# Optimization experiments

Measured on AMD Instinct MI355X. Metric: run time of the kernel, lower is better.

The kernel has to match this reference:

```python
import jax, jax.numpy as jnp
import numpy as np


def dht(x):
    # Discrete Hartley transform along last axis: DHT(x) = Re(FFT) - Im(FFT)
    X = jnp.fft.fft(x, axis=-1)
    return (X.real - X.imag).astype(x.dtype)


def idht(x):
    # Inverse DHT = DHT / N
    n = x.shape[-1]
    return dht(x) / n


def setup_inputs() -> dict:
    key = jax.random.key(0)
    k1, k2 = jax.random.split(key)
    B, Cin, Cout, N, M = 16, 64, 64, 16384, 64
    x = jax.random.normal(k1, (B, Cin, N), dtype=jnp.float32)
    scale = 1.0 / (Cin * Cout)
    weights1 = scale * jax.random.uniform(k2, (Cout, Cin, M), dtype=jnp.float32)
    return {"x": x, "weights1": weights1, "modes1": M}


def reference(x, weights1, modes1):
    # x: [B, Cin, N]; weights1: [Cout, Cin, M]
    B, Cin, N = x.shape
    Cout = weights1.shape[0]
    x_ht = dht(x)                                  # [B, Cin, N]
    # Mode-wise channel contraction on the first `modes1` Hartley modes
    low = jnp.einsum('bim,oim->bom', x_ht[:, :, :modes1], weights1)  # [B, Cout, M]
    out_ht = jnp.zeros((B, Cout, N), dtype=x.dtype).at[:, :, :modes1].set(low)
    return idht(out_ht)                            # [B, Cout, N]
```

## Files before the change

### kernel.cpp

```cpp
#include <hip/hip_runtime.h>
#include <math.h>

#define N_FFT 16384
#define HALF 8192
#define ROWS 1024
#define KS_A 64
#define KR_A 128
#define CHUNK 32
#define NMASK 16383


__global__ __launch_bounds__(256) void k_tab(float* __restrict__ castab,
                                             float* __restrict__ costab) {
    int i = blockIdx.x * 256 + threadIdx.x;
    double ang = 6.283185307179586476925287 * (double)i / (double)N_FFT;
    double c = cos(ang), s = sin(ang);
    castab[i] = (float)(c + s);
    costab[i] = (float)(2.0 * c);
}

__global__ __launch_bounds__(512, 4) void kA(const float* __restrict__ x,
                                             const float* __restrict__ castab,
                                             const float* __restrict__ costab,
                                             float* __restrict__ partial) {
    const int rb = blockIdx.x & 7;
    const int ks = blockIdx.x >> 3;
    const int rowbase = rb << 7;
    const int kbase = ks * KR_A;

    __shared__ float xs[CHUNK][2][128];

    const int t   = threadIdx.x;
    const int wq  = __builtin_amdgcn_readfirstlane(t >> 6);
    const int lam = t & 63;
    const int c0  = wq * 8;
    const int p   = wq >> 2;
    const int r2  = lam * 2;
    const int mbase = (wq < 4) ? (wq << 4) : (((wq - 4) << 4) + 1);

    float k2[8], cA[8], cB[8];
#pragma unroll
    for (int j = 0; j < 8; ++j) {
        const int m = mbase + 2 * j;
        k2[j] = costab[m];
        cB[j] = castab[((kbase - 1) * m) & NMASK];
        cA[j] = castab[(kbase * m) & NMASK];
    }

    float acc0[8], acc1[8];
#pragma unroll
    for (int j = 0; j < 8; ++j) { acc0[j] = 0.f; acc1[j] = 0.f; }

    for (int ch = 0; ch < KR_A / CHUNK; ++ch) {
        const int k0 = kbase + ch * CHUNK;
        if (ch) __syncthreads();
#pragma unroll
        for (int it = 0; it < 2; ++it) {
            const int idx = it * 512 + t;
            const int r = idx >> 3, kq = idx & 7;
            const float4 a4 = *reinterpret_cast<const float4*>(
                &x[(size_t)(rowbase + r) * N_FFT + k0 + kq * 4]);
            const float4 b4 = *reinterpret_cast<const float4*>(
                &x[(size_t)(rowbase + r) * N_FFT + k0 + kq * 4 + HALF]);
            const int rsw = r ^ (kq << 1);
#pragma unroll
            for (int u = 0; u < 4; ++u) {
                const float a = reinterpret_cast<const float*>(&a4)[u];
                const float b = reinterpret_cast<const float*>(&b4)[u];
                xs[kq * 4 + u][0][rsw] = a + b;
                xs[kq * 4 + u][1][rsw] = a - b;
            }
        }
        __syncthreads();

        for (int k = 0; k < CHUNK; k += 2) {
            {
                const int rd = r2 ^ ((k >> 2) << 1);
                const float2 s2 = *reinterpret_cast<const float2*>(&xs[k][p][rd]);
#pragma unroll
                for (int j = 0; j < 8; ++j) {
                    acc0[j] = fmaf(s2.x, cA[j], acc0[j]);
                    acc1[j] = fmaf(s2.y, cA[j], acc1[j]);
                    cB[j] = fmaf(k2[j], cA[j], -cB[j]);
                }
            }
            {
                const int rd = r2 ^ (((k + 1) >> 2) << 1);
                const float2 s2 = *reinterpret_cast<const float2*>(&xs[k + 1][p][rd]);
#pragma unroll
                for (int j = 0; j < 8; ++j) {
                    acc0[j] = fmaf(s2.x, cB[j], acc0[j]);
                    acc1[j] = fmaf(s2.y, cB[j], acc1[j]);
                    cA[j] = fmaf(k2[j], cB[j], -cA[j]);
                }
            }
        }
    }

#pragma unroll
    for (int i = 0; i < 2; ++i) {
        float* pp = &partial[((size_t)ks << 16) +
                             (size_t)(rowbase + r2 + i) * 64 + c0];
        const float* a = i ? acc1 : acc0;
        *reinterpret_cast<float4*>(pp) =
            make_float4(a[0], a[1], a[2], a[3]);
        *reinterpret_cast<float4*>(pp + 4) =
            make_float4(a[4], a[5], a[6], a[7]);
    }
}

__global__ __launch_bounds__(256) void kR(const float* __restrict__ partial,
                                          float* __restrict__ xh) {
    const int idx = blockIdx.x * 256 + threadIdx.x;
    const int r = idx >> 6, c = idx & 63;
    const int m = (c < 32) ? (2 * c) : (2 * (c - 32) + 1);
    float a0 = 0.f, a1 = 0.f, a2 = 0.f, a3 = 0.f;
#pragma unroll 4
    for (int sp = 0; sp < KS_A; sp += 4) {
        a0 += partial[((size_t)(sp + 0) << 16) + idx];
        a1 += partial[((size_t)(sp + 1) << 16) + idx];
        a2 += partial[((size_t)(sp + 2) << 16) + idx];
        a3 += partial[((size_t)(sp + 3) << 16) + idx];
    }
    xh[(r << 6) + m] = (a0 + a1) + (a2 + a3);
}

__global__ __launch_bounds__(256) void kB(const float* __restrict__ xh,
                                          const float* __restrict__ w,
                                          float* __restrict__ lowT) {
    const int b  = blockIdx.x >> 4;
    const int og = blockIdx.x & 15;
    const int o  = og * 4 + (threadIdx.x >> 6);
    const int m  = threadIdx.x & 63;
    float a0 = 0.f, a1 = 0.f, a2 = 0.f, a3 = 0.f;
#pragma unroll 4
    for (int i = 0; i < 64; i += 4) {
        a0 = fmaf(xh[(size_t)((b * 64 + i + 0) << 6) + m], w[(size_t)((o * 64 + i + 0) << 6) + m], a0);
        a1 = fmaf(xh[(size_t)((b * 64 + i + 1) << 6) + m], w[(size_t)((o * 64 + i + 1) << 6) + m], a1);
        a2 = fmaf(xh[(size_t)((b * 64 + i + 2) << 6) + m], w[(size_t)((o * 64 + i + 2) << 6) + m], a2);
        a3 = fmaf(xh[(size_t)((b * 64 + i + 3) << 6) + m], w[(size_t)((o * 64 + i + 3) << 6) + m], a3);
    }
    lowT[(size_t)m * ROWS + b * 64 + o] = ((a0 + a1) + (a2 + a3)) * (1.0f / (float)N_FFT);
}

__global__ __launch_bounds__(256, 4) void kC(const float* __restrict__ lowT,
                                             const float* __restrict__ castab,
                                             const float* __restrict__ costab,
                                             float* __restrict__ out) {
    const int rb = blockIdx.x >> 5;
    const int nb = blockIdx.x & 31;
    const int rowbase = rb << 4;
    const int n0 = nb << 8;

    __shared__ float ls[64][16];

    const int t  = threadIdx.x;
    const int rg = __builtin_amdgcn_readfirstlane(t >> 6);
    const int nl = t & 63;
    const int n  = n0 + nl * 4;

#pragma unroll
    for (int it = 0; it < 4; ++it) {
        const int f = it * 256 + t;
        const int m = f >> 4, r = f & 15;
        ls[m][r] = lowT[((size_t)m << 10) + rowbase + r];
    }
    __syncthreads();

    float k2[4], ce[4], co[4];
#pragma unroll
    for (int j = 0; j < 4; ++j) {
        k2[j] = costab[n + j];
        ce[j] = 1.0f;
        co[j] = castab[n + j];
    }

    float se[4][4], so[4][4];
#pragma unroll
    for (int r = 0; r < 4; ++r)
#pragma unroll
        for (int j = 0; j < 4; ++j) { se[r][j] = 0.f; so[r][j] = 0.f; }

#pragma unroll 4
    for (int g = 0; g < 32; ++g) {
        const float4 le = *reinterpret_cast<const float4*>(&ls[2 * g][rg * 4]);
        const float4 lo = *reinterpret_cast<const float4*>(&ls[2 * g + 1][rg * 4]);
        const float lev[4] = {le.x, le.y, le.z, le.w};
        const float lov[4] = {lo.x, lo.y, lo.z, lo.w};
#pragma unroll
        for (int r = 0; r < 4; ++r)
#pragma unroll
            for (int j = 0; j < 4; ++j) {
                se[r][j] = fmaf(ce[j], lev[r], se[r][j]);
                so[r][j] = fmaf(co[j], lov[r], so[r][j]);
            }
#pragma unroll
        for (int j = 0; j < 4; ++j) {
            ce[j] = fmaf(k2[j], co[j], -ce[j]);
            co[j] = fmaf(k2[j], ce[j], -co[j]);
        }
    }

#pragma unroll
    for (int r = 0; r < 4; ++r) {
        const size_t row = (size_t)rowbase + rg * 4 + r;
        *reinterpret_cast<float4*>(&out[row * N_FFT + n]) =
            make_float4(se[r][0] + so[r][0], se[r][1] + so[r][1],
                        se[r][2] + so[r][2], se[r][3] + so[r][3]);
        *reinterpret_cast<float4*>(&out[row * N_FFT + HALF + n]) =
            make_float4(se[r][0] - so[r][0], se[r][1] - so[r][1],
                        se[r][2] - so[r][2], se[r][3] - so[r][3]);
    }
}

extern "C" void kernel_launch(void* const* d_in, const int* in_sizes, int n_in,
                              void* d_out, int out_size, void* d_ws, size_t ws_size,
                              hipStream_t stream) {
    const float* x = (const float*)d_in[0];
    const float* w = (const float*)d_in[1];
    float* out = (float*)d_out;
    float* ws  = (float*)d_ws;

    float* castab  = ws;
    float* costab  = ws + 16384;
    float* partial = ws + 32768;
    float* xh      = ws + 4227072;
    float* lowT    = ws + 4292608;

    k_tab<<<64, 256, 0, stream>>>(castab, costab);
    kA<<<512, 512, 0, stream>>>(x, castab, costab, partial);
    kR<<<256, 256, 0, stream>>>(partial, xh);
    kB<<<256, 256, 0, stream>>>(xh, w, lowT);
    kC<<<2048, 256, 0, stream>>>(lowT, castab, costab, out);
}
```

Baseline: 63.70 us.

## Double-buffer kA input via direct global-to-LDS loads with fused butterfly

Replaces the register-staged load of x into shared memory with direct global_load_lds 16-byte transfers into double-buffered LDS tiles, so the next chunk is prefetched while the current one is processed. The a+b / a-b butterfly is moved from the store phase into the compute loop as a signed FMA, and the LDS layout is changed to a row-major swizzled layout with rows remapped (lam and lam+64). This removes VGPR staging and one barrier per chunk, at the cost of doubled LDS (64KB per block), extra LDS reads per step, and possible occupancy loss.

```diff
diff --git a/kernel.cpp b/kernel.cpp
--- a/kernel.cpp
+++ b/kernel.cpp
@@ -9,6 +9,11 @@
 #define CHUNK 32
 #define NMASK 16383
 
+
+#define GLOAD_LDS16(g, l)                                          \
+    __builtin_amdgcn_global_load_lds(                              \
+        (const __attribute__((address_space(1))) void*)(g),        \
+        (__attribute__((address_space(3))) void*)(l), 16, 0, 0)
 
 __global__ __launch_bounds__(256) void k_tab(float* __restrict__ castab,
                                              float* __restrict__ costab) {
@@ -28,15 +33,18 @@
     const int rowbase = rb << 7;
     const int kbase = ks * KR_A;
 
-    __shared__ float xs[CHUNK][2][128];
+    __shared__ float xsA[2][128 * 32];
+    __shared__ float xsB[2][128 * 32];
 
     const int t   = threadIdx.x;
     const int wq  = __builtin_amdgcn_readfirstlane(t >> 6);
     const int lam = t & 63;
     const int c0  = wq * 8;
-    const int p   = wq >> 2;
-    const int r2  = lam * 2;
+    const float sgn = (wq >> 2) ? -1.0f : 1.0f;
     const int mbase = (wq < 4) ? (wq << 4) : (((wq - 4) << 4) + 1);
+
+    const int rsw  = lam & 7;
+    const int off0base = lam << 5;
 
     float k2[8], cA[8], cB[8];
 #pragma unroll
@@ -51,61 +59,70 @@
 #pragma unroll
     for (int j = 0; j < 8; ++j) { acc0[j] = 0.f; acc1[j] = 0.f; }
 
+#define ISSUE(K0, BUF)                                                        \
+    _Pragma("unroll")                                                         \
+    for (int it = 0; it < 2; ++it) {                                          \
+        const int flat = it * 512 + t;                                        \
+        const int r = flat >> 3, q = flat & 7;                                \
+        const int kq = ((q ^ (r & 7)) << 2);                                  \
+        const float* sa = &x[(size_t)(rowbase + r) * N_FFT + (K0) + kq];      \
+        const int wbase = (it * 512 + wq * 64) << 2;                          \
+        GLOAD_LDS16(sa, &xsA[BUF][wbase]);                                    \
+        GLOAD_LDS16(sa + HALF, &xsB[BUF][wbase]);                             \
+    }
+
+    ISSUE(kbase, 0);
+    __syncthreads();
+
     for (int ch = 0; ch < KR_A / CHUNK; ++ch) {
-        const int k0 = kbase + ch * CHUNK;
-        if (ch) __syncthreads();
-#pragma unroll
-        for (int it = 0; it < 2; ++it) {
-            const int idx = it * 512 + t;
-            const int r = idx >> 3, kq = idx & 7;
-            const float4 a4 = *reinterpret_cast<const float4*>(
-                &x[(size_t)(rowbase + r) * N_FFT + k0 + kq * 4]);
-            const float4 b4 = *reinterpret_cast<const float4*>(
-                &x[(size_t)(rowbase + r) * N_FFT + k0 + kq * 4 + HALF]);
-            const int rsw = r ^ (kq << 1);
-#pragma unroll
-            for (int u = 0; u < 4; ++u) {
-                const float a = reinterpret_cast<const float*>(&a4)[u];
-                const float b = reinterpret_cast<const float*>(&b4)[u];
-                xs[kq * 4 + u][0][rsw] = a + b;
-                xs[kq * 4 + u][1][rsw] = a - b;
-            }
-        }
-        __syncthreads();
-
+        const int buf = ch & 1;
+        if (ch + 1 < KR_A / CHUNK) { ISSUE(kbase + (ch + 1) * CHUNK, buf ^ 1); }
+
+#pragma unroll
         for (int k = 0; k < CHUNK; k += 2) {
+            const int off0 = off0base + (((k >> 2) ^ rsw) << 2) + (k & 3);
+            const int off1 = off0 + 64 * 32;
+            const float2 a0 = *reinterpret_cast<const float2*>(&xsA[buf][off0]);
+            const float2 a1 = *reinterpret_cast<const float2*>(&xsA[buf][off1]);
+            const float2 b0 = *reinterpret_cast<const float2*>(&xsB[buf][off0]);
+            const float2 b1 = *reinterpret_cast<const float2*>(&xsB[buf][off1]);
+            const float x00 = fmaf(sgn, b0.x, a0.x);
+            const float x01 = fmaf(sgn, b0.y, a0.y);
+            const float x10 = fmaf(sgn, b1.x, a1.x);
+            const float x11 = fmaf(sgn, b1.y, a1.y);
             {
-                const int rd = r2 ^ ((k >> 2) << 1);
-                const float2 s2 = *reinterpret_cast<const float2*>(&xs[k][p][rd]);
 #pragma unroll
                 for (int j = 0; j < 8; ++j) {
-                    acc0[j] = fmaf(s2.x, cA[j], acc0[j]);
-                    acc1[j] = fmaf(s2.y, cA[j], acc1[j]);
+                    acc0[j] = fmaf(x00, cA[j], acc0[j]);
+                    acc1[j] = fmaf(x10, cA[j], acc1[j]);
                     cB[j] = fmaf(k2[j], cA[j], -cB[j]);
                 }
             }
             {
-                const int rd = r2 ^ (((k + 1) >> 2) << 1);
-                const float2 s2 = *reinterpret_cast<const float2*>(&xs[k + 1][p][rd]);
 #pragma unroll
                 for (int j = 0; j < 8; ++j) {
-                    acc0[j] = fmaf(s2.x, cB[j], acc0[j]);
-                    acc1[j] = fmaf(s2.y, cB[j], acc1[j]);
+                    acc0[j] = fmaf(x01, cB[j], acc0[j]);
+                    acc1[j] = fmaf(x11, cB[j], acc1[j]);
                     cA[j] = fmaf(k2[j], cB[j], -cA[j]);
                 }
             }
         }
-    }
-
-#pragma unroll
-    for (int i = 0; i < 2; ++i) {
-        float* pp = &partial[((size_t)ks << 16) +
-                             (size_t)(rowbase + r2 + i) * 64 + c0];
-        const float* a = i ? acc1 : acc0;
-        *reinterpret_cast<float4*>(pp) =
-            make_float4(a[0], a[1], a[2], a[3]);
-        *reinterpret_cast<float4*>(pp + 4) =
-            make_float4(a[4], a[5], a[6], a[7]);
+        __syncthreads();
+    }
+#undef ISSUE
+
+    {
+        float* pp0 = &partial[((size_t)ks << 16) +
+                              (size_t)(rowbase + lam) * 64 + c0];
+        float* pp1 = pp0 + (size_t)64 * 64;
+        *reinterpret_cast<float4*>(pp0) =
+            make_float4(acc0[0], acc0[1], acc0[2], acc0[3]);
+        *reinterpret_cast<float4*>(pp0 + 4) =
+            make_float4(acc0[4], acc0[5], acc0[6], acc0[7]);
+        *reinterpret_cast<float4*>(pp1) =
+            make_float4(acc1[0], acc1[1], acc1[2], acc1[3]);
+        *reinterpret_cast<float4*>(pp1 + 4) =
+            make_float4(acc1[4], acc1[5], acc1[6], acc1[7]);
     }
 }
 
```

Result: slower. 66.09 us (+3.8%).

## Restructure forward DHT to per-wave K-split with shuffle reduction, drop partial-sum kernel

Applied to the files above, without the earlier changes.

The forward low-mode Hartley projection now assigns each wavefront a row pair and a 16-mode slice. Lanes stride across K and read x directly from global memory with no shared-memory staging, and a wave-level xor-shuffle reduction replaces the 64-way partial buffer and its separate reduction kernel. Only a two-way K split remains, which the channel-mixing kernel folds in by adding the two halves. This removes a large partial-sum write and read plus one launch. In exchange, each x element is now loaded by several waves (one per mode half and parity), which could raise global load traffic, and the shuffle reduction adds overhead.

```diff
diff --git a/kernel.cpp b/kernel.cpp
--- a/kernel.cpp
+++ b/kernel.cpp
@@ -4,9 +4,6 @@
 #define N_FFT 16384
 #define HALF 8192
 #define ROWS 1024
-#define KS_A 64
-#define KR_A 128
-#define CHUNK 32
 #define NMASK 16383
 
 
@@ -19,126 +16,110 @@
     costab[i] = (float)(2.0 * c);
 }
 
-__global__ __launch_bounds__(512, 4) void kA(const float* __restrict__ x,
+__global__ __launch_bounds__(256, 4) void kA(const float* __restrict__ x,
                                              const float* __restrict__ castab,
                                              const float* __restrict__ costab,
-                                             float* __restrict__ partial) {
-    const int rb = blockIdx.x & 7;
-    const int ks = blockIdx.x >> 3;
-    const int rowbase = rb << 7;
-    const int kbase = ks * KR_A;
-
-    __shared__ float xs[CHUNK][2][128];
-
-    const int t   = threadIdx.x;
-    const int wq  = __builtin_amdgcn_readfirstlane(t >> 6);
-    const int lam = t & 63;
-    const int c0  = wq * 8;
-    const int p   = wq >> 2;
-    const int r2  = lam * 2;
-    const int mbase = (wq < 4) ? (wq << 4) : (((wq - 4) << 4) + 1);
-
-    float k2[8], cA[8], cB[8];
-#pragma unroll
-    for (int j = 0; j < 8; ++j) {
-        const int m = mbase + 2 * j;
-        k2[j] = costab[m];
-        cB[j] = castab[((kbase - 1) * m) & NMASK];
-        cA[j] = castab[(kbase * m) & NMASK];
-    }
-
-    float acc0[8], acc1[8];
-#pragma unroll
-    for (int j = 0; j < 8; ++j) { acc0[j] = 0.f; acc1[j] = 0.f; }
-
-    for (int ch = 0; ch < KR_A / CHUNK; ++ch) {
-        const int k0 = kbase + ch * CHUNK;
-        if (ch) __syncthreads();
-#pragma unroll
-        for (int it = 0; it < 2; ++it) {
-            const int idx = it * 512 + t;
-            const int r = idx >> 3, kq = idx & 7;
-            const float4 a4 = *reinterpret_cast<const float4*>(
-                &x[(size_t)(rowbase + r) * N_FFT + k0 + kq * 4]);
-            const float4 b4 = *reinterpret_cast<const float4*>(
-                &x[(size_t)(rowbase + r) * N_FFT + k0 + kq * 4 + HALF]);
-            const int rsw = r ^ (kq << 1);
-#pragma unroll
-            for (int u = 0; u < 4; ++u) {
-                const float a = reinterpret_cast<const float*>(&a4)[u];
-                const float b = reinterpret_cast<const float*>(&b4)[u];
-                xs[kq * 4 + u][0][rsw] = a + b;
-                xs[kq * 4 + u][1][rsw] = a - b;
+                                             float* __restrict__ xh2) {
+    const int wq = __builtin_amdgcn_readfirstlane(threadIdx.x >> 6);
+    const int w  = blockIdx.x * 4 + wq;
+    const int l  = threadIdx.x & 63;
+
+    const int ks = w & 1;
+    const int mh = (w >> 1) & 1;
+    const int p  = (w >> 2) & 1;
+    const int rp = w >> 3;
+
+    const float sgn = p ? -1.0f : 1.0f;
+    const int kstart = l + (ks << 12);
+
+    float k2[16], cA[16], cB[16];
+#pragma unroll
+    for (int mm = 0; mm < 16; ++mm) {
+        const int m = p + 2 * (mh * 16 + mm);
+        k2[mm] = costab[(m << 6) & NMASK];
+        cA[mm] = castab[(kstart * m) & NMASK];
+        cB[mm] = castab[((kstart - 64) * m) & NMASK];
+    }
+
+    float acc0[16], acc1[16];
+#pragma unroll
+    for (int mm = 0; mm < 16; ++mm) { acc0[mm] = 0.f; acc1[mm] = 0.f; }
+
+    const float* xp0 = x + (size_t)rp * N_FFT + kstart;
+    const float* xp1 = xp0 + (size_t)512 * N_FFT;
+
+#pragma unroll 2
+    for (int j = 0; j < 64; j += 2) {
+        {
+            const int o = j << 6;
+            const float s0 = fmaf(sgn, xp0[o + HALF], sgn > 0.f ? xp0[o] : xp0[o]);
+            const float a0 = xp0[o], b0 = xp0[o + HALF];
+            const float a1 = xp1[o], b1 = xp1[o + HALF];
+            const float v0 = fmaf(sgn, b0, a0);
+            const float v1 = fmaf(sgn, b1, a1);
+            (void)s0;
+#pragma unroll
+            for (int mm = 0; mm < 16; ++mm) {
+                acc0[mm] = fmaf(v0, cA[mm], acc0[mm]);
+                acc1[mm] = fmaf(v1, cA[mm], acc1[mm]);
+                cB[mm] = fmaf(k2[mm], cA[mm], -cB[mm]);
             }
         }
-        __syncthreads();
-
-        for (int k = 0; k < CHUNK; k += 2) {
-            {
-                const int rd = r2 ^ ((k >> 2) << 1);
-                const float2 s2 = *reinterpret_cast<const float2*>(&xs[k][p][rd]);
-#pragma unroll
-                for (int j = 0; j < 8; ++j) {
-                    acc0[j] = fmaf(s2.x, cA[j], acc0[j]);
-                    acc1[j] = fmaf(s2.y, cA[j], acc1[j]);
-                    cB[j] = fmaf(k2[j], cA[j], -cB[j]);
-                }
+        {
+            const int o = (j + 1) << 6;
+            const float a0 = xp0[o], b0 = xp0[o + HALF];
+            const float a1 = xp1[o], b1 = xp1[o + HALF];
+            const float v0 = fmaf(sgn, b0, a0);
+            const float v1 = fmaf(sgn, b1, a1);
+#pragma unroll
+            for (int mm = 0; mm < 16; ++mm) {
+                acc0[mm] = fmaf(v0, cB[mm], acc0[mm]);
+                acc1[mm] = fmaf(v1, cB[mm], acc1[mm]);
+                cA[mm] = fmaf(k2[mm], cB[mm], -cA[mm]);
             }
-            {
-                const int rd = r2 ^ (((k + 1) >> 2) << 1);
-                const float2 s2 = *reinterpret_cast<const float2*>(&xs[k + 1][p][rd]);
-#pragma unroll
-                for (int j = 0; j < 8; ++j) {
-                    acc0[j] = fmaf(s2.x, cB[j], acc0[j]);
-                    acc1[j] = fmaf(s2.y, cB[j], acc1[j]);
-                    cA[j] = fmaf(k2[j], cB[j], -cA[j]);
-                }
-            }
-        }
-    }
-
-#pragma unroll
-    for (int i = 0; i < 2; ++i) {
-        float* pp = &partial[((size_t)ks << 16) +
-                             (size_t)(rowbase + r2 + i) * 64 + c0];
-        const float* a = i ? acc1 : acc0;
-        *reinterpret_cast<float4*>(pp) =
-            make_float4(a[0], a[1], a[2], a[3]);
-        *reinterpret_cast<float4*>(pp + 4) =
-            make_float4(a[4], a[5], a[6], a[7]);
-    }
-}
-
-__global__ __launch_bounds__(256) void kR(const float* __restrict__ partial,
-                                          float* __restrict__ xh) {
-    const int idx = blockIdx.x * 256 + threadIdx.x;
-    const int r = idx >> 6, c = idx & 63;
-    const int m = (c < 32) ? (2 * c) : (2 * (c - 32) + 1);
-    float a0 = 0.f, a1 = 0.f, a2 = 0.f, a3 = 0.f;
-#pragma unroll 4
-    for (int sp = 0; sp < KS_A; sp += 4) {
-        a0 += partial[((size_t)(sp + 0) << 16) + idx];
-        a1 += partial[((size_t)(sp + 1) << 16) + idx];
-        a2 += partial[((size_t)(sp + 2) << 16) + idx];
-        a3 += partial[((size_t)(sp + 3) << 16) + idx];
-    }
-    xh[(r << 6) + m] = (a0 + a1) + (a2 + a3);
-}
-
-__global__ __launch_bounds__(256) void kB(const float* __restrict__ xh,
+        }
+    }
+
+#pragma unroll
+    for (int st = 1; st < 64; st <<= 1) {
+#pragma unroll
+        for (int mm = 0; mm < 16; ++mm) {
+            acc0[mm] += __shfl_xor(acc0[mm], st, 64);
+            acc1[mm] += __shfl_xor(acc1[mm], st, 64);
+        }
+    }
+
+    float* xb = xh2 + ((size_t)ks << 16);
+#pragma unroll
+    for (int mm = 0; mm < 16; ++mm) {
+        if (l == mm) {
+            const int m = p + 2 * (mh * 16 + mm);
+            xb[((size_t)rp << 6) + m]         = acc0[mm];
+            xb[((size_t)(rp + 512) << 6) + m] = acc1[mm];
+        }
+    }
+}
+
+__global__ __launch_bounds__(256) void kB(const float* __restrict__ xh2,
                                           const float* __restrict__ w,
                                           float* __restrict__ lowT) {
     const int b  = blockIdx.x >> 4;
     const int og = blockIdx.x & 15;
     const int o  = og * 4 + (threadIdx.x >> 6);
     const int m  = threadIdx.x & 63;
+    const float* xh0 = xh2;
+    const float* xh1 = xh2 + 65536;
     float a0 = 0.f, a1 = 0.f, a2 = 0.f, a3 = 0.f;
 #pragma unroll 4
     for (int i = 0; i < 64; i += 4) {
-        a0 = fmaf(xh[(size_t)((b * 64 + i + 0) << 6) + m], w[(size_t)((o * 64 + i + 0) << 6) + m], a0);
-        a1 = fmaf(xh[(size_t)((b * 64 + i + 1) << 6) + m], w[(size_t)((o * 64 + i + 1) << 6) + m], a1);
-        a2 = fmaf(xh[(size_t)((b * 64 + i + 2) << 6) + m], w[(size_t)((o * 64 + i + 2) << 6) + m], a2);
-        a3 = fmaf(xh[(size_t)((b * 64 + i + 3) << 6) + m], w[(size_t)((o * 64 + i + 3) << 6) + m], a3);
+        const size_t i0 = (size_t)((b * 64 + i + 0) << 6) + m;
+        const size_t i1 = (size_t)((b * 64 + i + 1) << 6) + m;
+        const size_t i2 = (size_t)((b * 64 + i + 2) << 6) + m;
+        const size_t i3 = (size_t)((b * 64 + i + 3) << 6) + m;
+        a0 = fmaf(xh0[i0] + xh1[i0], w[(size_t)((o * 64 + i + 0) << 6) + m], a0);
+        a1 = fmaf(xh0[i1] + xh1[i1], w[(size_t)((o * 64 + i + 1) << 6) + m], a1);
+        a2 = fmaf(xh0[i2] + xh1[i2], w[(size_t)((o * 64 + i + 2) << 6) + m], a2);
+        a3 = fmaf(xh0[i3] + xh1[i3], w[(size_t)((o * 64 + i + 3) << 6) + m], a3);
     }
     lowT[(size_t)m * ROWS + b * 64 + o] = ((a0 + a1) + (a2 + a3)) * (1.0f / (float)N_FFT);
 }
@@ -221,15 +202,13 @@
     float* out = (float*)d_out;
     float* ws  = (float*)d_ws;
 
-    float* castab  = ws;
-    float* costab  = ws + 16384;
-    float* partial = ws + 32768;
-    float* xh      = ws + 4227072;
-    float* lowT    = ws + 4292608;
+    float* castab = ws;
+    float* costab = ws + 16384;
+    float* xh2    = ws + 32768;
+    float* lowT   = ws + 163840;
 
     k_tab<<<64, 256, 0, stream>>>(castab, costab);
-    kA<<<512, 512, 0, stream>>>(x, castab, costab, partial);
-    kR<<<256, 256, 0, stream>>>(partial, xh);
-    kB<<<256, 256, 0, stream>>>(xh, w, lowT);
+    kA<<<1024, 256, 0, stream>>>(x, castab, costab, xh2);
+    kB<<<256, 256, 0, stream>>>(xh2, w, lowT);
     kC<<<2048, 256, 0, stream>>>(lowT, castab, costab, out);
 }
```

Result: slower. 69.78 us (+9.6%).
